# Kernel tuning notes

Hardware: AMD Instinct MI355X
Metric: run time of the kernel (lower is better)

The kernel has to match this reference:

```python
import jax, jax.numpy as jnp
from jax import lax
import numpy as np

# ---- module config (mirrors SSDDecodeLayer init kwargs) ----
IMG_H = 300.0
IMG_W = 300.0
CONF_THRESH = 0.5
IOU_THRESH = 0.45
TOP_K = 200
NMS_MAX = 100          # nms_max_output_size
NUM_CLASSES = 21       # incl. background (class 0, skipped in the loop)
NORMALIZE_COORDS = True
NEG = jnp.float32(-1e30)  # sentinel for suppressed / below-threshold scores


def setup_inputs() -> dict:
    key = jax.random.key(0)
    k1, k2, k3, k4 = jax.random.split(key, 4)
    B, N, C = 64, 8732, NUM_CLASSES
    conf = jax.random.uniform(k1, (B, N, C))                       # class confidences in [0,1]
    loc = jax.random.normal(k2, (B, N, 4)) * 0.1                   # encoded box offsets
    cxcy = jax.random.uniform(k3, (B, N, 2))                       # anchor centers in [0,1]
    wh = jax.random.uniform(k4, (B, N, 2), minval=0.05, maxval=0.3)  # anchor sizes
    var = jnp.broadcast_to(jnp.array([0.1, 0.1, 0.2, 0.2], jnp.float32), (B, N, 4))
    prediction = jnp.concatenate([conf, loc, cxcy, wh, var], axis=-1).astype(jnp.float32)
    return {"prediction": prediction}  # [B, N, NUM_CLASSES + 12]


def _decode(prediction):
    """SSD box decode: offsets * variance * anchor -> corner coords."""
    C = prediction.shape[-1] - 12
    conf = prediction[..., :C]
    loc = prediction[..., C:C + 4]
    anc = prediction[..., C + 4:C + 8]
    var = prediction[..., C + 8:]
    cx = loc[..., 0] * var[..., 0] * anc[..., 2] + anc[..., 0]
    cy = loc[..., 1] * var[..., 1] * anc[..., 3] + anc[..., 1]
    w = jnp.exp(loc[..., 2] * var[..., 2]) * anc[..., 2]
    h = jnp.exp(loc[..., 3] * var[..., 3]) * anc[..., 3]
    xmin = cx - 0.5 * w
    ymin = cy - 0.5 * h
    xmax = cx + 0.5 * w
    ymax = cy + 0.5 * h
    if NORMALIZE_COORDS:
        xmin = xmin * IMG_W
        xmax = xmax * IMG_W
        ymin = ymin * IMG_H
        ymax = ymax * IMG_H
    boxes = jnp.stack([xmin, ymin, xmax, ymax], axis=-1)  # [B, N, 4]
    return conf, boxes


def _iou_one_vs_all(box, boxes):
    """IoU of a single box [4] vs boxes [N,4] (xmin,ymin,xmax,ymax)."""
    ix0 = jnp.maximum(box[0], boxes[:, 0])
    iy0 = jnp.maximum(box[1], boxes[:, 1])
    ix1 = jnp.minimum(box[2], boxes[:, 2])
    iy1 = jnp.minimum(box[3], boxes[:, 3])
    inter = jnp.maximum(ix1 - ix0, 0.0) * jnp.maximum(iy1 - iy0, 0.0)
    a1 = jnp.maximum(box[2] - box[0], 0.0) * jnp.maximum(box[3] - box[1], 0.0)
    a2 = jnp.maximum(boxes[:, 2] - boxes[:, 0], 0.0) * jnp.maximum(boxes[:, 3] - boxes[:, 1], 0.0)
    return inter / jnp.maximum(a1 + a2 - inter, 1e-8)


def _greedy_nms(boxes, scores):
    """Fixed-shape greedy NMS: returns (indices [NMS_MAX], valid [NMS_MAX]).
    Matches tf.image.non_max_suppression semantics (suppress IoU > threshold)
    after the score > CONF_THRESH boolean mask."""
    s0 = jnp.where(scores > CONF_THRESH, scores, NEG)

    def step(s, _):
        best = jnp.argmax(s)
        ok = s[best] > NEG * 0.5      # still a real (unsuppressed, above-thresh) box
        iou = _iou_one_vs_all(boxes[best], boxes)
        s = jnp.where(iou > IOU_THRESH, NEG, s)  # suppresses best itself (IoU=1)
        return s, (best, ok)

    _, (idx, ok) = lax.scan(step, s0, None, length=NMS_MAX)
    return idx, ok


def _per_image(conf, boxes):
    """conf [N, C], boxes [N, 4] -> [TOP_K, 6] rows of (class_id, score, xmin, ymin, xmax, ymax)."""
    dtype = conf.dtype
    cls_ids = jnp.arange(1, conf.shape[-1], dtype=dtype)  # skip background class 0
    cls_scores = conf[:, 1:].T                            # [C-1, N]

    def per_class(cid, scores):
        idx, ok = _greedy_nms(boxes, scores)
        okf = ok.astype(dtype)[:, None]
        rows = jnp.concatenate(
            [jnp.full((NMS_MAX, 1), cid, dtype=dtype),
             scores[idx][:, None],
             boxes[idx]], axis=-1) * okf                  # zero-pad invalid slots
        return rows                                       # [NMS_MAX, 6]

    rows = jax.vmap(per_class)(cls_ids, cls_scores)       # [C-1, NMS_MAX, 6]
    flat = rows.reshape(-1, 6)                            # [(C-1)*NMS_MAX, 6]
    _, tk_idx = lax.top_k(flat[:, 1], TOP_K)              # top-k by confidence
    return flat[tk_idx]                                   # [TOP_K, 6]


def reference(prediction):
    conf, boxes = _decode(prediction)
    return jax.vmap(_per_image)(conf, boxes)              # [B, TOP_K, 6]
```

## Files before the change

### kernel.cpp

```cpp
#include <hip/hip_runtime.h>
#include <math.h>


#pragma clang fp contract(off)

#define NANCH 8732
#define NB 64
#define NCLS 20
#define NMSMAX 100
#define TOPK 200
#define PRED_STRIDE 33
#define NTHR 512
#define NE 18
#define NBUCK 2048
#define NEGF -1e30f

__device__ __forceinline__ unsigned flipf(float f) {
  unsigned u = __float_as_uint(f);
  return u ^ ((u >> 31) ? 0xFFFFFFFFu : 0x80000000u);
}

__device__ __forceinline__ float unflipf(unsigned se) {
  unsigned sbits = (se & 0x80000000u) ? (se ^ 0x80000000u) : ~se;
  return __uint_as_float(sbits);
}

__device__ __forceinline__ int bucket_of(float s) {
  float t = (s - 0.5f) * 4096.0f;
  int b = (int)t;
  b = b < 0 ? 0 : (b > (NBUCK - 1) ? (NBUCK - 1) : b);
  return (NBUCK - 1) - b;
}

__device__ __forceinline__ bool iou_gt(float inter, float den) {
  const double THR = (double)0.45f + 0x1.0p-26;
  return (double)inter > THR * (double)den;
}

__device__ __forceinline__ float rdlanef(float v, int l) {
  return __uint_as_float(__builtin_amdgcn_readlane(__float_as_uint(v), l));
}

__global__ void decode_kernel(const float* __restrict__ pred,
                              float* __restrict__ boxes,
                              float* __restrict__ scores_t) {
#pragma clang fp contract(off)
  int n = blockIdx.x * blockDim.x + threadIdx.x;
  int b = blockIdx.y;
  if (n >= NANCH) return;
  long long idx = (long long)b * NANCH + n;
  const float* row = pred + idx * PRED_STRIDE;

  float l0 = row[21], l1 = row[22], l2 = row[23], l3 = row[24];
  float ax = row[25], ay = row[26], aw = row[27], ah = row[28];
  float v0 = row[29], v1 = row[30], v2 = row[31], v3 = row[32];

  float cx = (l0 * v0) * aw + ax;
  float cy = (l1 * v1) * ah + ay;
  float e2 = (float)exp((double)(l2 * v2));
  float e3 = (float)exp((double)(l3 * v3));
  float w = e2 * aw;
  float h = e3 * ah;
  float hw = 0.5f * w, hh = 0.5f * h;
  float xmin = (cx - hw) * 300.0f;
  float ymin = (cy - hh) * 300.0f;
  float xmax = (cx + hw) * 300.0f;
  float ymax = (cy + hh) * 300.0f;

  *(float4*)(boxes + idx * 4) = make_float4(xmin, ymin, xmax, ymax);

  if (scores_t) {
#pragma unroll
    for (int c = 0; c < NCLS; ++c) {
      scores_t[((long long)b * NCLS + c) * NANCH + n] = row[1 + c];
    }
  }
}

__global__ __launch_bounds__(NTHR) void nms_kernel(
    const float* __restrict__ boxes,
    const float* __restrict__ scores_t,
    const float* __restrict__ pred,
    float* __restrict__ rows) {
#pragma clang fp contract(off)
  const int g = blockIdx.x;
  const int b = g / NCLS;
  const int c1 = g % NCLS;
  const int tid = threadIdx.x;
  const int lane = tid & 63;
  const int wid = tid >> 6;

  __shared__ unsigned long long keys[NANCH];
  __shared__ unsigned off[NBUCK];
  __shared__ unsigned wsum[8];
  __shared__ float4 accb[NMSMAX];
  __shared__ float acca[NMSMAX];
  __shared__ int nacc_s;

  const float* bimg = boxes + (long long)b * NANCH * 4;
  float* grow = rows + (long long)g * NMSMAX * 6;

  for (int q = 0; q < NBUCK / NTHR; ++q) off[tid + q * NTHR] = 0u;
  __syncthreads();

  unsigned sflip[NE];
  short bkt[NE];
#pragma unroll
  for (int k = 0; k < NE; ++k) {
    int i = tid + (k << 9);
    bkt[k] = -1;
    if (i < NANCH) {
      float s = scores_t
          ? scores_t[((long long)b * NCLS + c1) * NANCH + i]
          : pred[((long long)b * NANCH + i) * PRED_STRIDE + 1 + c1];
      if (s > 0.5f) {
        int bb = bucket_of(s);
        bkt[k] = (short)bb;
        sflip[k] = flipf(s);
        atomicAdd(&off[bb], 1u);
      }
    }
  }
  __syncthreads();

  {
    unsigned v0 = off[(tid << 2) + 0], v1 = off[(tid << 2) + 1];
    unsigned v2 = off[(tid << 2) + 2], v3 = off[(tid << 2) + 3];
    unsigned ls = v0 + v1 + v2 + v3;
    unsigned x = ls;
#pragma unroll
    for (int d = 1; d < 64; d <<= 1) {
      unsigned y = __shfl_up(x, d);
      if (lane >= d) x += y;
    }
    if (lane == 63) wsum[wid] = x;
    __syncthreads();
    unsigned wbase = 0;
    for (int w = 0; w < wid; ++w) wbase += wsum[w];
    unsigned base = wbase + x - ls;
    off[(tid << 2) + 0] = base;
    off[(tid << 2) + 1] = base + v0;
    off[(tid << 2) + 2] = base + v0 + v1;
    off[(tid << 2) + 3] = base + v0 + v1 + v2;
  }
  __syncthreads();

#pragma unroll
  for (int k = 0; k < NE; ++k) {
    if (bkt[k] >= 0) {
      int i = tid + (k << 9);
      unsigned long long key = ((unsigned long long)sflip[k] << 32) |
                               (unsigned)(0xFFFFFFFFu - (unsigned)i);
      unsigned slot = atomicAdd(&off[(int)bkt[k]], 1u);
      keys[slot] = key;
    }
  }
  __syncthreads();

  for (int q = 0; q < NBUCK / NTHR; ++q) {
    int bk = tid * (NBUCK / NTHR) + q;
    int st = bk ? (int)off[bk - 1] : 0;
    int en = (int)off[bk];
    for (int i = st + 1; i < en; ++i) {
      unsigned long long k = keys[i];
      int j = i - 1;
      while (j >= st && keys[j] < k) { keys[j + 1] = keys[j]; --j; }
      keys[j + 1] = k;
    }
  }
  __syncthreads();

  const int ncand = (int)off[NBUCK - 1];

  if (wid == 0 && ncand > 0) {
    const float fcls = (float)(c1 + 1);
    int nacc = 0;
    const int nchunk = (ncand + 63) >> 6;

    int slot0 = lane < ncand ? lane : 0;
    unsigned long long kcur = keys[slot0];
    float4 cbv;
    {
      unsigned bidx = 0xFFFFFFFFu - (unsigned)(kcur & 0xFFFFFFFFu);
      cbv = *(const float4*)(bimg + (long long)bidx * 4);
    }

    for (int c = 0; c < nchunk && nacc < NMSMAX; ++c) {
      unsigned long long knxt = 0ull;
      float4 cbn = make_float4(0.f, 0.f, 0.f, 0.f);
      if (c + 1 < nchunk) {
        int sl = ((c + 1) << 6) + lane;
        int cl = sl < ncand ? sl : 0;
        knxt = keys[cl];
        unsigned bidx = 0xFFFFFFFFu - (unsigned)(knxt & 0xFFFFFFFFu);
        cbn = *(const float4*)(bimg + (long long)bidx * 4);
      }

      const float4 cb = cbv;
      const float ca = fmaxf(cb.z - cb.x, 0.f) * fmaxf(cb.w - cb.y, 0.f);
      bool su = ((c << 6) + lane) >= ncand;

      for (int j = 0; j < nacc; ++j) {
        float4 ab = accb[j];
        float aa = acca[j];
        float ix0 = fmaxf(ab.x, cb.x), iy0 = fmaxf(ab.y, cb.y);
        float ix1 = fminf(ab.z, cb.z), iy1 = fminf(ab.w, cb.w);
        float inter = fmaxf(ix1 - ix0, 0.f) * fmaxf(iy1 - iy0, 0.f);
        float den = fmaxf((aa + ca) - inter, 1e-8f);
        su = su || iou_gt(inter, den);
      }

      unsigned long long live = __ballot(!su);
      while (live && nacc < NMSMAX) {
        int l = __ffsll(live) - 1;
        float bx = rdlanef(cb.x, l), by = rdlanef(cb.y, l);
        float bz = rdlanef(cb.z, l), bw = rdlanef(cb.w, l);
        unsigned khi = __builtin_amdgcn_readlane((unsigned)(kcur >> 32), l);
        float aa = fmaxf(bz - bx, 0.f) * fmaxf(bw - by, 0.f);
        if (lane == 0) {
          float* gr = grow + nacc * 6;
          gr[0] = fcls;
          gr[1] = unflipf(khi);
          gr[2] = bx; gr[3] = by; gr[4] = bz; gr[5] = bw;
          accb[nacc] = make_float4(bx, by, bz, bw);
          acca[nacc] = aa;
        }
        ++nacc;
        float ix0 = fmaxf(bx, cb.x), iy0 = fmaxf(by, cb.y);
        float ix1 = fminf(bz, cb.z), iy1 = fminf(bw, cb.w);
        float inter = fmaxf(ix1 - ix0, 0.f) * fmaxf(iy1 - iy0, 0.f);
        float den = fmaxf((aa + ca) - inter, 1e-8f);
        su = su || iou_gt(inter, den) || (lane == l);
        live = __ballot(!su);
      }

      kcur = knxt; cbv = cbn;
    }
    if (lane == 0) nacc_s = nacc;
  } else if (tid == 0 && ncand == 0) {
    nacc_s = 0;
  }
  __syncthreads();

  for (int j = nacc_s * 6 + tid; j < NMSMAX * 6; j += NTHR) grow[j] = 0.f;
}

__global__ __launch_bounds__(512) void topk_kernel(const float* __restrict__ rows,
                                                   float* __restrict__ out) {
  __shared__ unsigned long long key[2048];
  const int b = blockIdx.x;
  const int tid = threadIdx.x;
  const float* rb = rows + (long long)b * (NCLS * NMSMAX) * 6;

  for (int e = tid; e < 2048; e += 512) {
    unsigned long long k = 0ull;
    if (e < NCLS * NMSMAX) {
      float s = rb[e * 6 + 1];
      unsigned se = flipf(s);
      k = ((unsigned long long)se << 32) | (unsigned)(0xFFFFFFFFu - (unsigned)e);
    }
    key[e] = k;
  }
  __syncthreads();

  for (unsigned k2 = 2; k2 <= 2048; k2 <<= 1) {
    for (unsigned j = k2 >> 1; j > 0; j >>= 1) {
      for (unsigned t = tid; t < 1024; t += 512) {
        unsigned i = t + (t & ~(j - 1));
        unsigned l = i + j;
        bool up = ((i & k2) == 0);
        unsigned long long a = key[i], c = key[l];
        if (up ? (a < c) : (a > c)) { key[i] = c; key[l] = a; }
      }
      __syncthreads();
    }
  }

  if (tid < TOPK) {
    unsigned long long kk = key[tid];
    unsigned e = 0xFFFFFFFFu - (unsigned)(kk & 0xFFFFFFFFu);
    const float* src = rb + (long long)e * 6;
    float* dst = out + ((long long)b * TOPK + tid) * 6;
#pragma unroll
    for (int j = 0; j < 6; ++j) dst[j] = src[j];
  }
}

extern "C" void kernel_launch(void* const* d_in, const int* in_sizes, int n_in,
                              void* d_out, int out_size, void* d_ws, size_t ws_size,
                              hipStream_t stream) {
  const float* pred = (const float*)d_in[0];
  float* out = (float*)d_out;
  float* ws = (float*)d_ws;

  const long long boxes_f = (long long)NB * NANCH * 4;
  const long long rows_f  = (long long)NB * NCLS * NMSMAX * 6;
  const long long st_f    = (long long)NB * NCLS * NANCH;

  float* boxes = ws;
  float* rows  = ws + boxes_f;
  float* st    = ws + boxes_f + rows_f;
  size_t need_st = (size_t)(boxes_f + rows_f + st_f) * sizeof(float);
  float* scores_t = (ws_size >= need_st) ? st : nullptr;

  dim3 dgrid((NANCH + 255) / 256, NB);
  decode_kernel<<<dgrid, 256, 0, stream>>>(pred, boxes, scores_t);
  nms_kernel<<<NB * NCLS, NTHR, 0, stream>>>(boxes, scores_t, pred, rows);
  topk_kernel<<<NB, 512, 0, stream>>>(rows, out);
}
```

Before: 278.9 us.

## Split NMS into sort and single-wave scan kernels, tile decode through LDS

```diff
diff --git a/kernel.cpp b/kernel.cpp
--- a/kernel.cpp
+++ b/kernel.cpp
@@ -14,6 +14,7 @@
 #define NE 18
 #define NBUCK 2048
 #define NEGF -1e30f
+#define DTILE 64
 
 __device__ __forceinline__ unsigned flipf(float f) {
   unsigned u = __float_as_uint(f);
@@ -41,43 +42,242 @@
   return __uint_as_float(__builtin_amdgcn_readlane(__float_as_uint(v), l));
 }
 
-__global__ void decode_kernel(const float* __restrict__ pred,
-                              float* __restrict__ boxes,
-                              float* __restrict__ scores_t) {
+__global__ __launch_bounds__(256) void decode_kernel(
+    const float* __restrict__ pred,
+    float* __restrict__ boxes,
+    float* __restrict__ scores_t) {
 #pragma clang fp contract(off)
-  int n = blockIdx.x * blockDim.x + threadIdx.x;
-  int b = blockIdx.y;
-  if (n >= NANCH) return;
-  long long idx = (long long)b * NANCH + n;
-  const float* row = pred + idx * PRED_STRIDE;
-
-  float l0 = row[21], l1 = row[22], l2 = row[23], l3 = row[24];
-  float ax = row[25], ay = row[26], aw = row[27], ah = row[28];
-  float v0 = row[29], v1 = row[30], v2 = row[31], v3 = row[32];
-
-  float cx = (l0 * v0) * aw + ax;
-  float cy = (l1 * v1) * ah + ay;
-  float e2 = (float)exp((double)(l2 * v2));
-  float e3 = (float)exp((double)(l3 * v3));
-  float w = e2 * aw;
-  float h = e3 * ah;
-  float hw = 0.5f * w, hh = 0.5f * h;
-  float xmin = (cx - hw) * 300.0f;
-  float ymin = (cy - hh) * 300.0f;
-  float xmax = (cx + hw) * 300.0f;
-  float ymax = (cy + hh) * 300.0f;
-
-  *(float4*)(boxes + idx * 4) = make_float4(xmin, ymin, xmax, ymax);
+  const int b = blockIdx.y;
+  const int n0 = blockIdx.x * DTILE;
+  const int na = (NANCH - n0) < DTILE ? (NANCH - n0) : DTILE;
+  const int tid = threadIdx.x;
+  const int l = tid & 63;
+
+  __shared__ float lds[DTILE * PRED_STRIDE];
+
+  const float* src = pred + ((long long)b * NANCH + n0) * PRED_STRIDE;
+  const int tot = na * PRED_STRIDE;
+  for (int e = tid; e < tot; e += 256) lds[e] = src[e];
+  __syncthreads();
+
+  if (tid < 64 && l < na) {
+    const float* row = lds + l * PRED_STRIDE;
+    float l0 = row[21], l1 = row[22], l2 = row[23], l3 = row[24];
+    float ax = row[25], ay = row[26], aw = row[27], ah = row[28];
+    float v0 = row[29], v1 = row[30], v2 = row[31], v3 = row[32];
+
+    float cx = (l0 * v0) * aw + ax;
+    float cy = (l1 * v1) * ah + ay;
+    float e2 = (float)exp((double)(l2 * v2));
+    float e3 = (float)exp((double)(l3 * v3));
+    float w = e2 * aw;
+    float h = e3 * ah;
+    float hw = 0.5f * w, hh = 0.5f * h;
+    float xmin = (cx - hw) * 300.0f;
+    float ymin = (cy - hh) * 300.0f;
+    float xmax = (cx + hw) * 300.0f;
+    float ymax = (cy + hh) * 300.0f;
+    *(float4*)(boxes + ((long long)b * NANCH + n0 + l) * 4) =
+        make_float4(xmin, ymin, xmax, ymax);
+  }
 
   if (scores_t) {
 #pragma unroll
-    for (int c = 0; c < NCLS; ++c) {
-      scores_t[((long long)b * NCLS + c) * NANCH + n] = row[1 + c];
-    }
-  }
-}
-
-__global__ __launch_bounds__(NTHR) void nms_kernel(
+    for (int it = 0; it < 5; ++it) {
+      int c = (tid >> 6) + (it << 2);
+      if (l < na) {
+        scores_t[((long long)b * NCLS + c) * NANCH + n0 + l] =
+            lds[l * PRED_STRIDE + 1 + c];
+      }
+    }
+  }
+}
+
+__global__ __launch_bounds__(NTHR) void sort_kernel(
+    const float* __restrict__ scores_t,
+    unsigned short* __restrict__ sidx,
+    int* __restrict__ ncand_g) {
+#pragma clang fp contract(off)
+  const int g = blockIdx.x;
+  const int b = g / NCLS;
+  const int c1 = g % NCLS;
+  const int tid = threadIdx.x;
+  const int lane = tid & 63;
+  const int wid = tid >> 6;
+
+  __shared__ unsigned long long keys[NANCH];
+  __shared__ unsigned off[NBUCK];
+  __shared__ unsigned wsum[8];
+
+  const float* srow = scores_t + ((long long)b * NCLS + c1) * NANCH;
+
+  for (int q = 0; q < NBUCK / NTHR; ++q) off[tid + q * NTHR] = 0u;
+  __syncthreads();
+
+  unsigned sflip[NE];
+  short bkt[NE];
+#pragma unroll
+  for (int k = 0; k < NE; ++k) {
+    int i = tid + (k << 9);
+    bkt[k] = -1;
+    if (i < NANCH) {
+      float s = srow[i];
+      if (s > 0.5f) {
+        int bb = bucket_of(s);
+        bkt[k] = (short)bb;
+        sflip[k] = flipf(s);
+        atomicAdd(&off[bb], 1u);
+      }
+    }
+  }
+  __syncthreads();
+
+  {
+    unsigned v0 = off[(tid << 2) + 0], v1 = off[(tid << 2) + 1];
+    unsigned v2 = off[(tid << 2) + 2], v3 = off[(tid << 2) + 3];
+    unsigned ls = v0 + v1 + v2 + v3;
+    unsigned x = ls;
+#pragma unroll
+    for (int d = 1; d < 64; d <<= 1) {
+      unsigned y = __shfl_up(x, d);
+      if (lane >= d) x += y;
+    }
+    if (lane == 63) wsum[wid] = x;
+    __syncthreads();
+    unsigned wbase = 0;
+    for (int w = 0; w < wid; ++w) wbase += wsum[w];
+    unsigned base = wbase + x - ls;
+    off[(tid << 2) + 0] = base;
+    off[(tid << 2) + 1] = base + v0;
+    off[(tid << 2) + 2] = base + v0 + v1;
+    off[(tid << 2) + 3] = base + v0 + v1 + v2;
+  }
+  __syncthreads();
+
+#pragma unroll
+  for (int k = 0; k < NE; ++k) {
+    if (bkt[k] >= 0) {
+      int i = tid + (k << 9);
+      unsigned long long key = ((unsigned long long)sflip[k] << 32) |
+                               (unsigned)(0xFFFFFFFFu - (unsigned)i);
+      unsigned slot = atomicAdd(&off[(int)bkt[k]], 1u);
+      keys[slot] = key;
+    }
+  }
+  __syncthreads();
+
+  for (int q = 0; q < NBUCK / NTHR; ++q) {
+    int bk = tid * (NBUCK / NTHR) + q;
+    int st = bk ? (int)off[bk - 1] : 0;
+    int en = (int)off[bk];
+    for (int i = st + 1; i < en; ++i) {
+      unsigned long long k = keys[i];
+      int j = i - 1;
+      while (j >= st && keys[j] < k) { keys[j + 1] = keys[j]; --j; }
+      keys[j + 1] = k;
+    }
+  }
+  __syncthreads();
+
+  const int ncand = (int)off[NBUCK - 1];
+
+  unsigned short* sg = sidx + (long long)g * NANCH;
+  for (int s = tid; s < ncand; s += NTHR) {
+    sg[s] = (unsigned short)(0xFFFFFFFFu - (unsigned)(keys[s] & 0xFFFFFFFFu));
+  }
+  if (tid == 0) ncand_g[g] = ncand;
+}
+
+__global__ __launch_bounds__(64) void scan_kernel(
+    const float* __restrict__ boxes,
+    const float* __restrict__ scores_t,
+    const unsigned short* __restrict__ sidx,
+    const int* __restrict__ ncand_g,
+    float* __restrict__ rows) {
+#pragma clang fp contract(off)
+  const int g = blockIdx.x;
+  const int b = g / NCLS;
+  const int c1 = g % NCLS;
+  const int lane = threadIdx.x;
+
+  __shared__ float4 accb[NMSMAX];
+  __shared__ float acca[NMSMAX];
+
+  const float* bimg = boxes + (long long)b * NANCH * 4;
+  const float* srow = scores_t + ((long long)b * NCLS + c1) * NANCH;
+  const unsigned short* sg = sidx + (long long)g * NANCH;
+  float* grow = rows + (long long)g * NMSMAX * 6;
+
+  const int ncand = ncand_g[g];
+  int nacc = 0;
+
+  if (ncand > 0) {
+    const float fcls = (float)(c1 + 1);
+    const int nchunk = (ncand + 63) >> 6;
+
+    int cl0 = lane < ncand ? lane : ncand - 1;
+    unsigned id0 = sg[cl0];
+    float4 cbv = *(const float4*)(bimg + (long long)id0 * 4);
+    float scv = srow[id0];
+
+    for (int c = 0; c < nchunk && nacc < NMSMAX; ++c) {
+      float4 cbn = make_float4(0.f, 0.f, 0.f, 0.f);
+      float scn = 0.f;
+      if (c + 1 < nchunk) {
+        int sl = ((c + 1) << 6) + lane;
+        int cl = sl < ncand ? sl : ncand - 1;
+        unsigned id = sg[cl];
+        cbn = *(const float4*)(bimg + (long long)id * 4);
+        scn = srow[id];
+      }
+
+      const float4 cb = cbv;
+      const float sc = scv;
+      const float ca = fmaxf(cb.z - cb.x, 0.f) * fmaxf(cb.w - cb.y, 0.f);
+      bool su = ((c << 6) + lane) >= ncand;
+
+      for (int j = 0; j < nacc; ++j) {
+        float4 ab = accb[j];
+        float aa = acca[j];
+        float ix0 = fmaxf(ab.x, cb.x), iy0 = fmaxf(ab.y, cb.y);
+        float ix1 = fminf(ab.z, cb.z), iy1 = fminf(ab.w, cb.w);
+        float inter = fmaxf(ix1 - ix0, 0.f) * fmaxf(iy1 - iy0, 0.f);
+        float den = fmaxf((aa + ca) - inter, 1e-8f);
+        su = su || iou_gt(inter, den);
+      }
+
+      unsigned long long live = __ballot(!su);
+      while (live && nacc < NMSMAX) {
+        int l = __ffsll(live) - 1;
+        float bx = rdlanef(cb.x, l), by = rdlanef(cb.y, l);
+        float bz = rdlanef(cb.z, l), bw = rdlanef(cb.w, l);
+        float bs = rdlanef(sc, l);
+        float aa = fmaxf(bz - bx, 0.f) * fmaxf(bw - by, 0.f);
+        if (lane == 0) {
+          float* gr = grow + nacc * 6;
+          gr[0] = fcls;
+          gr[1] = bs;
+          gr[2] = bx; gr[3] = by; gr[4] = bz; gr[5] = bw;
+          accb[nacc] = make_float4(bx, by, bz, bw);
+          acca[nacc] = aa;
+        }
+        ++nacc;
+        float ix0 = fmaxf(bx, cb.x), iy0 = fmaxf(by, cb.y);
+        float ix1 = fminf(bz, cb.z), iy1 = fminf(bw, cb.w);
+        float inter = fmaxf(ix1 - ix0, 0.f) * fmaxf(iy1 - iy0, 0.f);
+        float den = fmaxf((aa + ca) - inter, 1e-8f);
+        su = su || iou_gt(inter, den) || (lane == l);
+        live = __ballot(!su);
+      }
+
+      cbv = cbn; scv = scn;
+    }
+  }
+
+  for (int j = nacc * 6 + lane; j < NMSMAX * 6; j += 64) grow[j] = 0.f;
+}
+
+__global__ __launch_bounds__(NTHR) void nms_fused_kernel(
     const float* __restrict__ boxes,
     const float* __restrict__ scores_t,
     const float* __restrict__ pred,
@@ -296,15 +496,30 @@
   const long long boxes_f = (long long)NB * NANCH * 4;
   const long long rows_f  = (long long)NB * NCLS * NMSMAX * 6;
   const long long st_f    = (long long)NB * NCLS * NANCH;
+  const long long sidx_f  = (long long)NB * NCLS * NANCH / 2;
+  const long long ncand_f = NB * NCLS;
 
   float* boxes = ws;
   float* rows  = ws + boxes_f;
   float* st    = ws + boxes_f + rows_f;
-  size_t need_st = (size_t)(boxes_f + rows_f + st_f) * sizeof(float);
-  float* scores_t = (ws_size >= need_st) ? st : nullptr;
-
-  dim3 dgrid((NANCH + 255) / 256, NB);
+  unsigned short* sidx = (unsigned short*)(ws + boxes_f + rows_f + st_f);
+  int* ncand = (int*)(ws + boxes_f + rows_f + st_f + sidx_f);
+
+  size_t need_scores = (size_t)(boxes_f + rows_f + st_f) * sizeof(float);
+  size_t need_full   = (size_t)(boxes_f + rows_f + st_f + sidx_f + ncand_f) * sizeof(float);
+
+  bool have_scores = ws_size >= need_scores;
+  bool full = ws_size >= need_full;
+  float* scores_t = have_scores ? st : nullptr;
+
+  dim3 dgrid((NANCH + DTILE - 1) / DTILE, NB);
   decode_kernel<<<dgrid, 256, 0, stream>>>(pred, boxes, scores_t);
-  nms_kernel<<<NB * NCLS, NTHR, 0, stream>>>(boxes, scores_t, pred, rows);
+
+  if (full) {
+    sort_kernel<<<NB * NCLS, NTHR, 0, stream>>>(scores_t, sidx, ncand);
+    scan_kernel<<<NB * NCLS, 64, 0, stream>>>(boxes, scores_t, sidx, ncand, rows);
+  } else {
+    nms_fused_kernel<<<NB * NCLS, NTHR, 0, stream>>>(boxes, scores_t, pred, rows);
+  }
   topk_kernel<<<NB, 512, 0, stream>>>(rows, out);
 }
```

Result: faster. 240.3 us (-13.8%).

## Stage decode rows through LDS and sort buckets lazily per NMS chunk

Applied to the files above, without the earlier changes.

```diff
diff --git a/kernel.cpp b/kernel.cpp
--- a/kernel.cpp
+++ b/kernel.cpp
@@ -13,7 +13,7 @@
 #define NTHR 512
 #define NE 18
 #define NBUCK 2048
-#define NEGF -1e30f
+#define DTILE 256
 
 __device__ __forceinline__ unsigned flipf(float f) {
   unsigned u = __float_as_uint(f);
@@ -41,43 +41,54 @@
   return __uint_as_float(__builtin_amdgcn_readlane(__float_as_uint(v), l));
 }
 
-__global__ void decode_kernel(const float* __restrict__ pred,
-                              float* __restrict__ boxes,
-                              float* __restrict__ scores_t) {
+__global__ __launch_bounds__(256) void decode_kernel(
+    const float* __restrict__ pred,
+    float* __restrict__ boxes,
+    float* __restrict__ scores_t) {
 #pragma clang fp contract(off)
-  int n = blockIdx.x * blockDim.x + threadIdx.x;
-  int b = blockIdx.y;
-  if (n >= NANCH) return;
-  long long idx = (long long)b * NANCH + n;
-  const float* row = pred + idx * PRED_STRIDE;
-
-  float l0 = row[21], l1 = row[22], l2 = row[23], l3 = row[24];
-  float ax = row[25], ay = row[26], aw = row[27], ah = row[28];
-  float v0 = row[29], v1 = row[30], v2 = row[31], v3 = row[32];
-
-  float cx = (l0 * v0) * aw + ax;
-  float cy = (l1 * v1) * ah + ay;
-  float e2 = (float)exp((double)(l2 * v2));
-  float e3 = (float)exp((double)(l3 * v3));
-  float w = e2 * aw;
-  float h = e3 * ah;
-  float hw = 0.5f * w, hh = 0.5f * h;
-  float xmin = (cx - hw) * 300.0f;
-  float ymin = (cy - hh) * 300.0f;
-  float xmax = (cx + hw) * 300.0f;
-  float ymax = (cy + hh) * 300.0f;
-
-  *(float4*)(boxes + idx * 4) = make_float4(xmin, ymin, xmax, ymax);
-
-  if (scores_t) {
+  const int b = blockIdx.y;
+  const int n0 = blockIdx.x * DTILE;
+  const int na = (NANCH - n0) < DTILE ? (NANCH - n0) : DTILE;
+  const int tid = threadIdx.x;
+
+  __shared__ float lds[DTILE * PRED_STRIDE];
+
+  const float* src = pred + ((long long)b * NANCH + n0) * PRED_STRIDE;
+  const int tot = na * PRED_STRIDE;
+  for (int e = tid; e < tot; e += 256) lds[e] = src[e];
+  __syncthreads();
+
+  if (tid < na) {
+    const float* row = lds + tid * PRED_STRIDE;
+    float l0 = row[21], l1 = row[22], l2 = row[23], l3 = row[24];
+    float ax = row[25], ay = row[26], aw = row[27], ah = row[28];
+    float v0 = row[29], v1 = row[30], v2 = row[31], v3 = row[32];
+
+    float cx = (l0 * v0) * aw + ax;
+    float cy = (l1 * v1) * ah + ay;
+    float e2 = (float)exp((double)(l2 * v2));
+    float e3 = (float)exp((double)(l3 * v3));
+    float w = e2 * aw;
+    float h = e3 * ah;
+    float hw = 0.5f * w, hh = 0.5f * h;
+    float xmin = (cx - hw) * 300.0f;
+    float ymin = (cy - hh) * 300.0f;
+    float xmax = (cx + hw) * 300.0f;
+    float ymax = (cy + hh) * 300.0f;
+    *(float4*)(boxes + ((long long)b * NANCH + n0 + tid) * 4) =
+        make_float4(xmin, ymin, xmax, ymax);
+  }
+
+  if (scores_t && tid < na) {
 #pragma unroll
     for (int c = 0; c < NCLS; ++c) {
-      scores_t[((long long)b * NCLS + c) * NANCH + n] = row[1 + c];
-    }
-  }
-}
-
-__global__ __launch_bounds__(NTHR) void nms_kernel(
+      scores_t[((long long)b * NCLS + c) * NANCH + n0 + tid] =
+          lds[tid * PRED_STRIDE + 1 + c];
+    }
+  }
+}
+
+__global__ __launch_bounds__(NTHR) void nms_fused_kernel(
     const float* __restrict__ boxes,
     const float* __restrict__ scores_t,
     const float* __restrict__ pred,
@@ -96,11 +107,13 @@
   __shared__ float4 accb[NMSMAX];
   __shared__ float acca[NMSMAX];
   __shared__ int nacc_s;
+  __shared__ int maxb_s;
 
   const float* bimg = boxes + (long long)b * NANCH * 4;
   float* grow = rows + (long long)g * NMSMAX * 6;
 
   for (int q = 0; q < NBUCK / NTHR; ++q) off[tid + q * NTHR] = 0u;
+  if (tid == 0) maxb_s = 0;
   __syncthreads();
 
   unsigned sflip[NE];
@@ -126,6 +139,10 @@
   {
     unsigned v0 = off[(tid << 2) + 0], v1 = off[(tid << 2) + 1];
     unsigned v2 = off[(tid << 2) + 2], v3 = off[(tid << 2) + 3];
+    unsigned mv = v0 > v1 ? v0 : v1;
+    unsigned mv2 = v2 > v3 ? v2 : v3;
+    mv = mv > mv2 ? mv : mv2;
+    if (mv > 64u) atomicMax(&maxb_s, (int)mv);
     unsigned ls = v0 + v1 + v2 + v3;
     unsigned x = ls;
 #pragma unroll
@@ -157,88 +174,166 @@
   }
   __syncthreads();
 
-  for (int q = 0; q < NBUCK / NTHR; ++q) {
-    int bk = tid * (NBUCK / NTHR) + q;
-    int st = bk ? (int)off[bk - 1] : 0;
-    int en = (int)off[bk];
-    for (int i = st + 1; i < en; ++i) {
-      unsigned long long k = keys[i];
-      int j = i - 1;
-      while (j >= st && keys[j] < k) { keys[j + 1] = keys[j]; --j; }
-      keys[j + 1] = k;
-    }
-  }
-  __syncthreads();
-
   const int ncand = (int)off[NBUCK - 1];
-
-  if (wid == 0 && ncand > 0) {
+  const bool fastp = (maxb_s == 0);
+
+  if (!fastp) {
+    for (int q = 0; q < NBUCK / NTHR; ++q) {
+      int bk = tid * (NBUCK / NTHR) + q;
+      int st = bk ? (int)off[bk - 1] : 0;
+      int en = (int)off[bk];
+      for (int i = st + 1; i < en; ++i) {
+        unsigned long long k = keys[i];
+        int j = i - 1;
+        while (j >= st && keys[j] < k) { keys[j + 1] = keys[j]; --j; }
+        keys[j + 1] = k;
+      }
+    }
+    __syncthreads();
+  }
+
+  if (wid == 0) {
     const float fcls = (float)(c1 + 1);
     int nacc = 0;
-    const int nchunk = (ncand + 63) >> 6;
-
-    int slot0 = lane < ncand ? lane : 0;
-    unsigned long long kcur = keys[slot0];
-    float4 cbv;
-    {
-      unsigned bidx = 0xFFFFFFFFu - (unsigned)(kcur & 0xFFFFFFFFu);
-      cbv = *(const float4*)(bimg + (long long)bidx * 4);
-    }
-
-    for (int c = 0; c < nchunk && nacc < NMSMAX; ++c) {
-      unsigned long long knxt = 0ull;
-      float4 cbn = make_float4(0.f, 0.f, 0.f, 0.f);
-      if (c + 1 < nchunk) {
-        int sl = ((c + 1) << 6) + lane;
-        int cl = sl < ncand ? sl : 0;
-        knxt = keys[cl];
-        unsigned bidx = 0xFFFFFFFFu - (unsigned)(knxt & 0xFFFFFFFFu);
-        cbn = *(const float4*)(bimg + (long long)bidx * 4);
-      }
-
-      const float4 cb = cbv;
-      const float ca = fmaxf(cb.z - cb.x, 0.f) * fmaxf(cb.w - cb.y, 0.f);
-      bool su = ((c << 6) + lane) >= ncand;
-
-      for (int j = 0; j < nacc; ++j) {
-        float4 ab = accb[j];
-        float aa = acca[j];
-        float ix0 = fmaxf(ab.x, cb.x), iy0 = fmaxf(ab.y, cb.y);
-        float ix1 = fminf(ab.z, cb.z), iy1 = fminf(ab.w, cb.w);
-        float inter = fmaxf(ix1 - ix0, 0.f) * fmaxf(iy1 - iy0, 0.f);
-        float den = fmaxf((aa + ca) - inter, 1e-8f);
-        su = su || iou_gt(inter, den);
-      }
-
-      unsigned long long live = __ballot(!su);
-      while (live && nacc < NMSMAX) {
-        int l = __ffsll(live) - 1;
-        float bx = rdlanef(cb.x, l), by = rdlanef(cb.y, l);
-        float bz = rdlanef(cb.z, l), bw = rdlanef(cb.w, l);
-        unsigned khi = __builtin_amdgcn_readlane((unsigned)(kcur >> 32), l);
-        float aa = fmaxf(bz - bx, 0.f) * fmaxf(bw - by, 0.f);
-        if (lane == 0) {
-          float* gr = grow + nacc * 6;
-          gr[0] = fcls;
-          gr[1] = unflipf(khi);
-          gr[2] = bx; gr[3] = by; gr[4] = bz; gr[5] = bw;
-          accb[nacc] = make_float4(bx, by, bz, bw);
-          acca[nacc] = aa;
-        }
-        ++nacc;
-        float ix0 = fmaxf(bx, cb.x), iy0 = fmaxf(by, cb.y);
-        float ix1 = fminf(bz, cb.z), iy1 = fminf(bw, cb.w);
-        float inter = fmaxf(ix1 - ix0, 0.f) * fmaxf(iy1 - iy0, 0.f);
-        float den = fmaxf((aa + ca) - inter, 1e-8f);
-        su = su || iou_gt(inter, den) || (lane == l);
-        live = __ballot(!su);
-      }
-
-      kcur = knxt; cbv = cbn;
-    }
+
+    if (ncand > 0 && fastp) {
+      int s0 = 0, bcur = 0;
+      while (s0 < ncand && nacc < NMSMAX) {
+        int bend = bcur;
+        while (true) {
+          int bi = bend + lane;
+          bool ok = false;
+          if (bi < NBUCK) ok = (off[bi] - (unsigned)s0) <= 64u;
+          unsigned long long bal = __ballot(ok);
+          int cnt = __popcll(bal);
+          if (cnt == 64 && bend + 64 < NBUCK) { bend += 64; continue; }
+          bend += cnt;
+          break;
+        }
+        int send = (int)off[bend - 1];
+        int csz = send - s0;
+        bcur = bend;
+        if (csz == 0) { s0 = send; continue; }
+
+        unsigned long long v = (lane < csz) ? keys[s0 + lane] : 0ull;
+#pragma unroll
+        for (int k = 2; k <= 64; k <<= 1) {
+#pragma unroll
+          for (int j = k >> 1; j >= 1; j >>= 1) {
+            unsigned long long o = __shfl_xor(v, j);
+            bool keep_max = (((lane & k) == 0) == ((lane & j) == 0));
+            v = keep_max ? (v >= o ? v : o) : (v >= o ? o : v);
+          }
+        }
+
+        float4 cb = make_float4(0.f, 0.f, 0.f, 0.f);
+        if (lane < csz) {
+          unsigned bidx = 0xFFFFFFFFu - (unsigned)(v & 0xFFFFFFFFu);
+          cb = *(const float4*)(bimg + (long long)bidx * 4);
+        }
+        const float ca = fmaxf(cb.z - cb.x, 0.f) * fmaxf(cb.w - cb.y, 0.f);
+        bool su = lane >= csz;
+
+        for (int j = 0; j < nacc; ++j) {
+          float4 ab = accb[j];
+          float aa = acca[j];
+          float ix0 = fmaxf(ab.x, cb.x), iy0 = fmaxf(ab.y, cb.y);
+          float ix1 = fminf(ab.z, cb.z), iy1 = fminf(ab.w, cb.w);
+          float inter = fmaxf(ix1 - ix0, 0.f) * fmaxf(iy1 - iy0, 0.f);
+          float den = fmaxf((aa + ca) - inter, 1e-8f);
+          su = su || iou_gt(inter, den);
+        }
+
+        unsigned long long live = __ballot(!su);
+        while (live && nacc < NMSMAX) {
+          int l = __ffsll(live) - 1;
+          float bx = rdlanef(cb.x, l), by = rdlanef(cb.y, l);
+          float bz = rdlanef(cb.z, l), bw = rdlanef(cb.w, l);
+          unsigned khi = __builtin_amdgcn_readlane((unsigned)(v >> 32), l);
+          float aa = fmaxf(bz - bx, 0.f) * fmaxf(bw - by, 0.f);
+          if (lane == 0) {
+            float* gr = grow + nacc * 6;
+            gr[0] = fcls;
+            gr[1] = unflipf(khi);
+            gr[2] = bx; gr[3] = by; gr[4] = bz; gr[5] = bw;
+            accb[nacc] = make_float4(bx, by, bz, bw);
+            acca[nacc] = aa;
+          }
+          ++nacc;
+          float ix0 = fmaxf(bx, cb.x), iy0 = fmaxf(by, cb.y);
+          float ix1 = fminf(bz, cb.z), iy1 = fminf(bw, cb.w);
+          float inter = fmaxf(ix1 - ix0, 0.f) * fmaxf(iy1 - iy0, 0.f);
+          float den = fmaxf((aa + ca) - inter, 1e-8f);
+          su = su || iou_gt(inter, den) || (lane == l);
+          live = __ballot(!su);
+        }
+
+        s0 = send;
+      }
+    } else if (ncand > 0) {
+      const int nchunk = (ncand + 63) >> 6;
+      int slot0 = lane < ncand ? lane : 0;
+      unsigned long long kcur = keys[slot0];
+      float4 cbv;
+      {
+        unsigned bidx = 0xFFFFFFFFu - (unsigned)(kcur & 0xFFFFFFFFu);
+        cbv = *(const float4*)(bimg + (long long)bidx * 4);
+      }
+
+      for (int c = 0; c < nchunk && nacc < NMSMAX; ++c) {
+        unsigned long long knxt = 0ull;
+        float4 cbn = make_float4(0.f, 0.f, 0.f, 0.f);
+        if (c + 1 < nchunk) {
+          int sl = ((c + 1) << 6) + lane;
+          int cl = sl < ncand ? sl : 0;
+          knxt = keys[cl];
+          unsigned bidx = 0xFFFFFFFFu - (unsigned)(knxt & 0xFFFFFFFFu);
+          cbn = *(const float4*)(bimg + (long long)bidx * 4);
+        }
+
+        const float4 cb = cbv;
+        const float ca = fmaxf(cb.z - cb.x, 0.f) * fmaxf(cb.w - cb.y, 0.f);
+        bool su = ((c << 6) + lane) >= ncand;
+
+        for (int j = 0; j < nacc; ++j) {
+          float4 ab = accb[j];
+          float aa = acca[j];
+          float ix0 = fmaxf(ab.x, cb.x), iy0 = fmaxf(ab.y, cb.y);
+          float ix1 = fminf(ab.z, cb.z), iy1 = fminf(ab.w, cb.w);
+          float inter = fmaxf(ix1 - ix0, 0.f) * fmaxf(iy1 - iy0, 0.f);
+          float den = fmaxf((aa + ca) - inter, 1e-8f);
+          su = su || iou_gt(inter, den);
+        }
+
+        unsigned long long live = __ballot(!su);
+        while (live && nacc < NMSMAX) {
+          int l = __ffsll(live) - 1;
+          float bx = rdlanef(cb.x, l), by = rdlanef(cb.y, l);
+          float bz = rdlanef(cb.z, l), bw = rdlanef(cb.w, l);
+          unsigned khi = __builtin_amdgcn_readlane((unsigned)(kcur >> 32), l);
+          float aa = fmaxf(bz - bx, 0.f) * fmaxf(bw - by, 0.f);
+          if (lane == 0) {
+            float* gr = grow + nacc * 6;
+            gr[0] = fcls;
+            gr[1] = unflipf(khi);
+            gr[2] = bx; gr[3] = by; gr[4] = bz; gr[5] = bw;
+            accb[nacc] = make_float4(bx, by, bz, bw);
+            acca[nacc] = aa;
+          }
+          ++nacc;
+          float ix0 = fmaxf(bx, cb.x), iy0 = fmaxf(by, cb.y);
+          float ix1 = fminf(bz, cb.z), iy1 = fminf(bw, cb.w);
+          float inter = fmaxf(ix1 - ix0, 0.f) * fmaxf(iy1 - iy0, 0.f);
+          float den = fmaxf((aa + ca) - inter, 1e-8f);
+          su = su || iou_gt(inter, den) || (lane == l);
+          live = __ballot(!su);
+        }
+
+        kcur = knxt; cbv = cbn;
+      }
+    }
+
     if (lane == 0) nacc_s = nacc;
-  } else if (tid == 0 && ncand == 0) {
-    nacc_s = 0;
   }
   __syncthreads();
 
@@ -300,11 +395,11 @@
   float* boxes = ws;
   float* rows  = ws + boxes_f;
   float* st    = ws + boxes_f + rows_f;
-  size_t need_st = (size_t)(boxes_f + rows_f + st_f) * sizeof(float);
-  float* scores_t = (ws_size >= need_st) ? st : nullptr;
-
-  dim3 dgrid((NANCH + 255) / 256, NB);
+  size_t need_scores = (size_t)(boxes_f + rows_f + st_f) * sizeof(float);
+  float* scores_t = (ws_size >= need_scores) ? st : nullptr;
+
+  dim3 dgrid((NANCH + DTILE - 1) / DTILE, NB);
   decode_kernel<<<dgrid, 256, 0, stream>>>(pred, boxes, scores_t);
-  nms_kernel<<<NB * NCLS, NTHR, 0, stream>>>(boxes, scores_t, pred, rows);
+  nms_fused_kernel<<<NB * NCLS, NTHR, 0, stream>>>(boxes, scores_t, pred, rows);
   topk_kernel<<<NB, 512, 0, stream>>>(rows, out);
 }
```

New measurement: 262.6 us. 1.06x faster.
